# Performance work log

Measured on AMD Instinct MI355X. Metric: run time of the kernel, lower is better.

The kernel has to match this reference:

```python
import jax, jax.numpy as jnp
import numpy as np
from jax import lax

N = 10000
E = 320000
FLAT = 32 * 10 * 32  # conv channels * pooled 20x64 -> 10x32


def setup_inputs() -> dict:
    key = jax.random.key(0)
    ks = jax.random.split(key, 16)
    s = 0.05
    return {
        "features": jax.random.normal(ks[0], (N, 20, 64), jnp.float32),
        "src": jax.random.randint(ks[1], (E,), 0, N, jnp.int32),
        "dst": jax.random.randint(ks[2], (E,), 0, N, jnp.int32),
        # CNN params
        "conv_w": jax.random.normal(ks[3], (32, 1, 3, 3), jnp.float32) * s,
        "conv_b": jnp.zeros((32,), jnp.float32),
        "w1": jax.random.normal(ks[4], (FLAT, 32), jnp.float32) * s,
        "b1": jnp.zeros((32,), jnp.float32),
        "w2": jax.random.normal(ks[5], (32, 32), jnp.float32) * s,
        "b2": jnp.zeros((32,), jnp.float32),
        # SAGEConv1 (32 -> 64)
        "s1_self": jax.random.normal(ks[6], (32, 64), jnp.float32) * s,
        "s1_neigh": jax.random.normal(ks[7], (32, 64), jnp.float32) * s,
        "s1_b": jnp.zeros((64,), jnp.float32),
        # SAGEConv2 (64 -> 10)
        "s2_self": jax.random.normal(ks[8], (64, 10), jnp.float32) * s,
        "s2_neigh": jax.random.normal(ks[9], (64, 10), jnp.float32) * s,
        "s2_b": jnp.zeros((10,), jnp.float32),
    }


def _cnn(x, conv_w, conv_b, w1, b1, w2, b2):
    # x: [N, 1, 20, 64]
    x = lax.conv_general_dilated(x, conv_w, (1, 1), "SAME",
                                 dimension_numbers=("NCHW", "OIHW", "NCHW"))
    x = jax.nn.relu(x + conv_b[None, :, None, None])
    x = lax.reduce_window(x, -jnp.inf, lax.max, (1, 1, 2, 2), (1, 1, 2, 2), "VALID")
    x = x.reshape(x.shape[0], -1)  # [N, FLAT], NCHW flatten matches torch
    x = jax.nn.relu(x @ w1 + b1)
    x = jax.nn.relu(x @ w2 + b2)
    return x


def _sage_mean(x, src, dst, w_self, w_neigh, b):
    # DGL SAGEConv 'mean': mean over in-neighbors (messages src->dst)
    agg = jax.ops.segment_sum(x[src], dst, num_segments=N)
    deg = jax.ops.segment_sum(jnp.ones((src.shape[0],), x.dtype), dst, num_segments=N)
    agg = agg / jnp.maximum(deg, 1.0)[:, None]
    return x @ w_self + agg @ w_neigh + b


def reference(features, src, dst, conv_w, conv_b, w1, b1, w2, b2,
              s1_self, s1_neigh, s1_b, s2_self, s2_neigh, s2_b):
    h = _cnn(features[:, None, :, :], conv_w, conv_b, w1, b1, w2, b2)  # [N, 32]
    h = jax.nn.relu(_sage_mean(h, src, dst, s1_self, s1_neigh, s1_b))  # [N, 64]
    out = _sage_mean(h, src, dst, s2_self, s2_neigh, s2_b)             # [N, 10]
    return out
```

## Files before the change

kernel.cpp:

```cpp
#include <hip/hip_runtime.h>


typedef __attribute__((ext_vector_type(8)))  short bf16x8;
typedef __attribute__((ext_vector_type(4)))  float f32x4;
typedef __attribute__((ext_vector_type(16))) float f32x16;

__device__ __forceinline__ unsigned short f2bf(float v) {
    union { float f; unsigned int u; } x; x.f = v;
    unsigned int r = x.u + 0x7FFFu + ((x.u >> 16) & 1u);
    return (unsigned short)(r >> 16);
}
__device__ __forceinline__ float bf2f(unsigned short b) {
    union { float f; unsigned int u; } x; x.u = ((unsigned int)b) << 16;
    return x.f;
}
__device__ __forceinline__ unsigned cvtpk(float a, float b) {
    unsigned r;
    asm("v_cvt_pk_bf16_f32 %0, %1, %2" : "=v"(r) : "v"(a), "v"(b));
    return r;
}
__device__ __forceinline__ float lo2f(unsigned p) { union { unsigned u; float f; } x; x.u = p << 16; return x.f; }
__device__ __forceinline__ float hi2f(unsigned p) { union { unsigned u; float f; } x; x.u = p & 0xffff0000u; return x.f; }
__device__ __forceinline__ void split_pair(float a, float b, unsigned& hp, unsigned& lp) {
    hp = cvtpk(a, b);
    lp = cvtpk(a - lo2f(hp), b - hi2f(hp));
}

__global__ __launch_bounds__(256) void zero_ws(float* __restrict__ ws, int count) {
    int i = blockIdx.x * 256 + threadIdx.x;
    if (i < count) ws[i] = 0.0f;
}

__global__ __launch_bounds__(256) void w1_prep_v3(
    const float* __restrict__ w1, unsigned char* __restrict__ w1f)
{
    int gu = blockIdx.x * 256 + threadIdx.x;
    const int quarter = gu >> 11;
    const int u = gu & 2047;
    const int ph = quarter >> 2, qq = quarter & 3;
    const int ks   = u >> 8;
    const int jh   = (u >> 7) & 1;
    const int part = (u >> 6) & 1;
    const int lane = u & 63;
    const int j    = jh * 16 + (lane & 15);
    const int c    = ks * 4 + (lane >> 4);
    const int k0   = c * 320 + ph * 32 + qq * 8;
    unsigned short v[8];
#pragma unroll
    for (int i = 0; i < 8; ++i) {
        float x = w1[(size_t)(k0 + i) * 32 + j];
        unsigned short h = f2bf(x);
        v[i] = part ? f2bf(x - bf2f(h)) : h;
    }
    *(uint4*)(w1f + (size_t)quarter * 32768 + (size_t)u * 16) = *(const uint4*)v;
}

__global__ __launch_bounds__(256, 3) void cnn_fused_v10(
    const float* __restrict__ feat,
    const float* __restrict__ conv_w, const float* __restrict__ conv_b,
    const unsigned char* __restrict__ w1f,
    float* __restrict__ h_fc1)
{
    __shared__ __align__(16) unsigned char convA[18432];
    __shared__ __align__(16) unsigned char fc1A[32768];

    const int t = threadIdx.x;
    const int wv = t >> 6;
    const int lane = t & 63;
    const int base = blockIdx.x * 16;
    const int qq = blockIdx.y;

    const int nn  = lane >> 4;
    const int pwl = lane & 7;
    const int aa  = (lane >> 3) & 1;
    const float* featn = feat + (size_t)(base + wv * 4 + nn) * 1280;

    const int pw = qq * 8 + pwl;
    const int c0 = 2 * pw - 1;
    const bool cv0 = (c0 >= 0);
    const bool cv3 = (c0 + 3 < 64);

    const int cch = lane & 31;
    const int ckg = lane >> 5;
    const int rowr = lane & 31;
    unsigned rsw = (unsigned)(rowr << 4); rsw ^= ((rsw >> 7) & 3u) << 4;

    bf16x8 cbh, cbl;
    {
        union { unsigned short u[8]; bf16x8 v; } H, L;
#pragma unroll
        for (int i = 0; i < 8; ++i) {
            int k = ckg * 8 + i;
            float x = (k < 9) ? conv_w[cch * 9 + k] : 0.0f;
            unsigned short h = f2bf(x);
            H.u[i] = h; L.u[i] = f2bf(x - bf2f(h));
        }
        cbh = H.v; cbl = L.v;
    }
    const float cbias = conv_b[cch];

    const int nfr = lane & 15;

    f32x4 acc0 = {0.f, 0.f, 0.f, 0.f};
    f32x4 acc1 = {0.f, 0.f, 0.f, 0.f};
    const f32x16 czero = {};

    float f0[4], f1[4], f2[4], g1[4], g2[4];
    auto load_row = [&](int r, float* o) {
        bool rv = (r >= 0) && (r < 20);
        const float* rp = featn + (rv ? r : 0) * 64;
        float2 m = *(const float2*)(rp + c0 + 1);
        float v0 = rp[cv0 ? c0 : 0];
        float v3 = rp[cv3 ? (c0 + 3) : 0];
        o[0] = (rv && cv0) ? v0 : 0.f;
        o[1] = rv ? m.x : 0.f;
        o[2] = rv ? m.y : 0.f;
        o[3] = (rv && cv3) ? v3 : 0.f;
    };

    load_row(aa - 1, f0);
    load_row(aa,     f1);
    load_row(aa + 1, f2);
    load_row(aa + 2, g1);
    load_row(aa + 3, g2);

#pragma unroll
    for (int ph = 0; ph < 10; ++ph) {
        const int quarter = ph * 4 + qq;
        unsigned char* fbuf = fc1A + ((ph & 1) << 14);

        const unsigned char* wq = w1f + (size_t)quarter * 32768;
        bf16x8 bF[2][2][2];
#pragma unroll
        for (int si = 0; si < 2; ++si) {
            const int ks = wv + si * 4;
#pragma unroll
            for (int jh = 0; jh < 2; ++jh)
#pragma unroll
                for (int part = 0; part < 2; ++part)
                    bF[si][jh][part] = *(const bf16x8*)(
                        wq + (size_t)((((ks * 2 + jh) * 2 + part)) << 10) + lane * 16);
        }

        {
            unsigned P[3][2], Q[3][2];
            split_pair(f0[0], f0[1], P[0][0], Q[0][0]);
            split_pair(f0[2], f0[3], P[0][1], Q[0][1]);
            split_pair(f1[0], f1[1], P[1][0], Q[1][0]);
            split_pair(f1[2], f1[3], P[1][1], Q[1][1]);
            split_pair(f2[0], f2[1], P[2][0], Q[2][0]);
            split_pair(f2[2], f2[3], P[2][1], Q[2][1]);

            const int r0 = pwl * 4 + aa * 2, r1 = r0 + 1;
            unsigned b0 = (unsigned)(r0 << 4); b0 ^= ((b0 >> 7) & 3u) << 4;
            unsigned b1 = (unsigned)(r1 << 4); b1 ^= ((b1 >> 7) & 3u) << 4;
            unsigned char* abw = convA + ((wv * 4 + nn) << 10);
            uint4 H0 = make_uint4(P[0][0],
                                  __builtin_amdgcn_perm(P[1][0], P[0][1], 0x05040100u),
                                  __builtin_amdgcn_perm(P[1][1], P[1][0], 0x05040302u),
                                  P[2][0]);
            uint4 H1 = make_uint4(__builtin_amdgcn_perm(P[0][1], P[0][0], 0x05040302u),
                                  __builtin_amdgcn_perm(P[1][0], P[0][1], 0x07060302u),
                                  P[1][1],
                                  __builtin_amdgcn_perm(P[2][1], P[2][0], 0x05040302u));
            uint4 L0 = make_uint4(Q[0][0],
                                  __builtin_amdgcn_perm(Q[1][0], Q[0][1], 0x05040100u),
                                  __builtin_amdgcn_perm(Q[1][1], Q[1][0], 0x05040302u),
                                  Q[2][0]);
            uint4 L1 = make_uint4(__builtin_amdgcn_perm(Q[0][1], Q[0][0], 0x05040302u),
                                  __builtin_amdgcn_perm(Q[1][0], Q[0][1], 0x07060302u),
                                  Q[1][1],
                                  __builtin_amdgcn_perm(Q[2][1], Q[2][0], 0x05040302u));
            *(uint4*)(abw + b0)       = H0;
            *(uint4*)(abw + b1)       = H1;
            *(uint4*)(abw + 512 + b0) = L0;
            *(uint4*)(abw + 512 + b1) = L1;
            unsigned wr0 = __builtin_amdgcn_perm(Q[2][1], P[2][1], 0x05040100u);
            unsigned wr1 = __builtin_amdgcn_perm(Q[2][1], P[2][1], 0x07060302u);
            *(uint2*)(convA + 16384 + (((wv * 4 + nn) * 32 + r0) << 2)) = make_uint2(wr0, wr1);
        }

        if (ph < 9) {
#pragma unroll
            for (int j = 0; j < 4; ++j) { f0[j] = f2[j]; f1[j] = g1[j]; f2[j] = g2[j]; }
        }
        if (ph < 8) {
            load_row(2 * ph + 4 + aa, g1);
            load_row(2 * ph + 5 + aa, g2);
        }

#pragma unroll
        for (int nn2 = 0; nn2 < 4; ++nn2) {
            bf16x8 a_h, a_l;
            if (ckg == 0) {
                const unsigned char* ab = convA + ((wv * 4 + nn2) << 10);
                a_h = *(const bf16x8*)(ab + rsw);
                a_l = *(const bf16x8*)(ab + 512 + rsw);
            } else {
                unsigned cw = *(const unsigned*)(convA + 16384 + (((wv * 4 + nn2) * 32 + rowr) << 2));
                a_h = (bf16x8){(short)(cw & 0xffffu), 0, 0, 0, 0, 0, 0, 0};
                a_l = (bf16x8){(short)(cw >> 16),     0, 0, 0, 0, 0, 0, 0};
            }
            f32x16 ca;
            ca = __builtin_amdgcn_mfma_f32_32x32x16_bf16(a_l, cbh, czero, 0, 0, 0);
            ca = __builtin_amdgcn_mfma_f32_32x32x16_bf16(a_h, cbl, ca, 0, 0, 0);
            ca = __builtin_amdgcn_mfma_f32_32x32x16_bf16(a_h, cbh, ca, 0, 0, 0);

            float pv0 = fmaxf(fmaxf(fmaxf(ca[0],  ca[1]),  fmaxf(ca[2],  ca[3]))  + cbias, 0.f);
            float pv1 = fmaxf(fmaxf(fmaxf(ca[4],  ca[5]),  fmaxf(ca[6],  ca[7]))  + cbias, 0.f);
            float pv2 = fmaxf(fmaxf(fmaxf(ca[8],  ca[9]),  fmaxf(ca[10], ca[11])) + cbias, 0.f);
            float pv3 = fmaxf(fmaxf(fmaxf(ca[12], ca[13]), fmaxf(ca[14], ca[15])) + cbias, 0.f);

            unsigned ha, la, hb, lb;
            split_pair(pv0, pv1, ha, la);
            split_pair(pv2, pv3, hb, lb);
            unsigned pha = (unsigned)__shfl_xor((int)ha, 32);
            unsigned phb = (unsigned)__shfl_xor((int)hb, 32);
            unsigned pla = (unsigned)__shfl_xor((int)la, 32);
            unsigned plb = (unsigned)__shfl_xor((int)lb, 32);
            bool hih = (lane < 32);
            unsigned q0v = hih ? pha : la;
            unsigned q1v = hih ? ha  : pla;
            unsigned q2v = hih ? phb : lb;
            unsigned q3v = hih ? hb  : plb;
            unsigned w0  = __builtin_amdgcn_perm(q0v, q1v, 0x05040100u);
            unsigned w1v = __builtin_amdgcn_perm(q0v, q1v, 0x07060302u);
            unsigned w2v = __builtin_amdgcn_perm(q2v, q3v, 0x05040100u);
            unsigned w3v = __builtin_amdgcn_perm(q2v, q3v, 0x07060302u);
            const int nloc = wv * 4 + nn2;
            const int pS = hih ? 0 : 1;
            const int ksW = cch >> 2, kgW = cch & 3;
            unsigned byteW = (unsigned)((((pS * 8 + ksW) * 64) + kgW * 16 + nloc) << 4);
            byteW ^= ((byteW >> 8) & 7u) << 4;
            *(uint4*)(fbuf + byteW) = make_uint4(w0, w1v, w2v, w3v);
        }

        __syncthreads();

#pragma unroll
        for (int si = 0; si < 2; ++si) {
            const int ks = wv + si * 4;
            unsigned bH = (unsigned)(((0 * 8 + ks) << 10) + lane * 16); bH ^= ((bH >> 8) & 7u) << 4;
            unsigned bL = (unsigned)(((1 * 8 + ks) << 10) + lane * 16); bL ^= ((bL >> 8) & 7u) << 4;
            bf16x8 fa_h = *(const bf16x8*)(fbuf + bH);
            bf16x8 fa_l = *(const bf16x8*)(fbuf + bL);
            acc0 = __builtin_amdgcn_mfma_f32_16x16x32_bf16(fa_l, bF[si][0][0], acc0, 0, 0, 0);
            acc0 = __builtin_amdgcn_mfma_f32_16x16x32_bf16(fa_h, bF[si][0][1], acc0, 0, 0, 0);
            acc0 = __builtin_amdgcn_mfma_f32_16x16x32_bf16(fa_h, bF[si][0][0], acc0, 0, 0, 0);
            acc1 = __builtin_amdgcn_mfma_f32_16x16x32_bf16(fa_l, bF[si][1][0], acc1, 0, 0, 0);
            acc1 = __builtin_amdgcn_mfma_f32_16x16x32_bf16(fa_h, bF[si][1][1], acc1, 0, 0, 0);
            acc1 = __builtin_amdgcn_mfma_f32_16x16x32_bf16(fa_h, bF[si][1][0], acc1, 0, 0, 0);
        }
    }

    __syncthreads();
    float* red = (float*)convA;
#pragma unroll
    for (int r = 0; r < 4; ++r) {
        int node = (lane >> 4) * 4 + r;
        red[wv * 512 + node * 32 + nfr]      = acc0[r];
        red[wv * 512 + node * 32 + 16 + nfr] = acc1[r];
    }
    __syncthreads();
    {
        const int en = t >> 4, jp = t & 15;
        const int j0 = 2 * jp;
        float s0 = 0.f, s1 = 0.f;
#pragma unroll
        for (int wi = 0; wi < 4; ++wi) {
            s0 += red[wi * 512 + en * 32 + j0];
            s1 += red[wi * 512 + en * 32 + j0 + 1];
        }
        atomicAdd(&h_fc1[(size_t)(base + en) * 32 + j0],     s0);
        atomicAdd(&h_fc1[(size_t)(base + en) * 32 + j0 + 1], s1);
    }
}

__global__ __launch_bounds__(256) void fc1_finish(
    const float* __restrict__ h_fc1, const float* __restrict__ b1,
    const float* __restrict__ w2, const float* __restrict__ b2,
    float* __restrict__ h_out, int N)
{
    __shared__ float hr[8][32];
    const int t = threadIdx.x;
    const int nb = t >> 5, j = t & 31;
    const int n = blockIdx.x * 8 + nb;
    if (n < N) hr[nb][j] = fmaxf(h_fc1[(size_t)n * 32 + j] + b1[j], 0.f);
    __syncthreads();
    if (n >= N) return;
    float o = b2[j];
#pragma unroll
    for (int k = 0; k < 32; ++k) o = fmaf(hr[nb][k], w2[k * 32 + j], o);
    h_out[(size_t)n * 32 + j] = fmaxf(o, 0.f);
}

__global__ __launch_bounds__(256) void count_deg(
    const int* __restrict__ dst, int* __restrict__ cnt, int E)
{
    int e = blockIdx.x * 256 + threadIdx.x;
    if (e < E) atomicAdd(&cnt[dst[e]], 1);
}

__global__ __launch_bounds__(256) void scan_all(
    const int* __restrict__ cnt, int* __restrict__ row_ptr, int* __restrict__ cursor, int N)
{
    __shared__ int ps[256];
    const int t = threadIdx.x;
    const int base = t * 40;
    int vals[40];
    int run = 0;
#pragma unroll
    for (int i = 0; i < 40; ++i) {
        int idx = base + i;
        int v = (idx < N) ? cnt[idx] : 0;
        vals[i] = run;
        run += v;
    }
    ps[t] = run;
    __syncthreads();
#pragma unroll
    for (int off = 1; off < 256; off <<= 1) {
        int x = (t >= off) ? ps[t - off] : 0;
        __syncthreads();
        ps[t] += x;
        __syncthreads();
    }
    int excl = ps[t] - run;
#pragma unroll
    for (int i = 0; i < 40; ++i) {
        int idx = base + i;
        if (idx < N) {
            int rp = excl + vals[i];
            row_ptr[idx] = rp;
            cursor[idx]  = rp;
        }
    }
    if (t == 255) row_ptr[N] = ps[255];
}

__global__ __launch_bounds__(256) void fill_csr(
    const int* __restrict__ src, const int* __restrict__ dst,
    int* __restrict__ cursor, int* __restrict__ csr, int E)
{
    int e = blockIdx.x * 256 + threadIdx.x;
    if (e >= E) return;
    int idx = atomicAdd(&cursor[dst[e]], 1);
    csr[idx] = src[e];
}

__global__ __launch_bounds__(256) void sage1_fused(
    const float* __restrict__ h, const int* __restrict__ rp, const int* __restrict__ csr,
    const float* __restrict__ s1_self, const float* __restrict__ s1_neigh,
    const float* __restrict__ s1_b, const float* __restrict__ s2_neigh,
    float* __restrict__ h1, float* __restrict__ z16, int N)
{
    __shared__ float aggs[4][32];
    __shared__ float hl[4][64];
    const int t = threadIdx.x;
    const int nb = t >> 6, k = t & 63;
    const int n = blockIdx.x * 4 + nb;
    const int j = k & 31, half = k >> 5;

    int p0 = 0, p1 = 0;
    if (n < N) { p0 = rp[n]; p1 = rp[n + 1]; }
    float a = 0.f;
    for (int p = p0 + half; p < p1; p += 2)
        a += h[(size_t)csr[p] * 32 + j];
    a += __shfl_down(a, 32);
    if (half == 0) aggs[nb][j] = a;
    __syncthreads();

    float o = 0.f;
    if (n < N) {
        const int nu = __builtin_amdgcn_readfirstlane(n);
        float inv = 1.0f / fmaxf((float)(p1 - p0), 1.0f);
        o = s1_b[k];
#pragma unroll
        for (int jj = 0; jj < 32; ++jj) {
            o = fmaf(h[(size_t)nu * 32 + jj], s1_self[jj * 64 + k], o);
            o = fmaf(aggs[nb][jj] * inv, s1_neigh[jj * 64 + k], o);
        }
        o = fmaxf(o, 0.f);
        h1[(size_t)n * 64 + k] = o;
    }
    hl[nb][k] = o;
    __syncthreads();

    if (n < N && k < 16) {
        float z = 0.f;
        if (k < 10) {
#pragma unroll
            for (int jj = 0; jj < 64; ++jj) z = fmaf(hl[nb][jj], s2_neigh[jj * 10 + k], z);
        }
        z16[(size_t)n * 16 + k] = z;
    }
}

__global__ __launch_bounds__(256) void sage2_final_g(
    const float* __restrict__ h1, const float* __restrict__ z16,
    const int* __restrict__ rp, const int* __restrict__ csr,
    const float* __restrict__ s2_self, const float* __restrict__ s2_b,
    float* __restrict__ out, int N)
{
    int tid = blockIdx.x * 256 + threadIdx.x;
    int nn = tid >> 4, k = tid & 15;
    if (nn >= N || k >= 10) return;
    int p0 = rp[nn], p1 = rp[nn + 1];
    float a0 = 0.f, a1 = 0.f;
    int p = p0;
    for (; p + 2 <= p1; p += 2) {
        int s0 = csr[p], s1 = csr[p + 1];
        a0 += z16[(size_t)s0 * 16 + k];
        a1 += z16[(size_t)s1 * 16 + k];
    }
    if (p < p1) a0 += z16[(size_t)csr[p] * 16 + k];
    float inv = 1.0f / fmaxf((float)(p1 - p0), 1.0f);
    float o = s2_b[k] + (a0 + a1) * inv;
#pragma unroll
    for (int j = 0; j < 64; ++j) o = fmaf(h1[nn * 64 + j], s2_self[j * 10 + k], o);
    out[nn * 10 + k] = o;
}

extern "C" void kernel_launch(void* const* d_in, const int* in_sizes, int n_in,
                              void* d_out, int out_size, void* d_ws, size_t ws_size,
                              hipStream_t stream)
{
    const float* feat     = (const float*)d_in[0];
    const int*   src      = (const int*)d_in[1];
    const int*   dst      = (const int*)d_in[2];
    const float* conv_w   = (const float*)d_in[3];
    const float* conv_b   = (const float*)d_in[4];
    const float* w1       = (const float*)d_in[5];
    const float* b1       = (const float*)d_in[6];
    const float* w2       = (const float*)d_in[7];
    const float* b2       = (const float*)d_in[8];
    const float* s1_self  = (const float*)d_in[9];
    const float* s1_neigh = (const float*)d_in[10];
    const float* s1_b     = (const float*)d_in[11];
    const float* s2_self  = (const float*)d_in[12];
    const float* s2_neigh = (const float*)d_in[13];
    const float* s2_b     = (const float*)d_in[14];
    float* out = (float*)d_out;

    const int N = in_sizes[0] / 1280;
    const int E = in_sizes[1];

    char* wsb = (char*)d_ws;
    int*   row_cnt = (int*)wsb;                      wsb += (size_t)N * 4;
    float* h_fc1   = (float*)wsb;                    wsb += (size_t)N * 32 * 4;
    int*   row_ptr = (int*)wsb;                      wsb += (size_t)(N + 4) * 4;
    int*   cursor  = (int*)wsb;                      wsb += (size_t)N * 4;
    int*   csr     = (int*)wsb;                      wsb += (size_t)E * 4;
    float* h_cnn   = (float*)wsb;                    wsb += (size_t)N * 32 * 4;
    float* h1      = (float*)wsb;                    wsb += (size_t)N * 64 * 4;
    float* z16     = (float*)wsb;                    wsb += (size_t)N * 16 * 4;
    unsigned char* w1f = (unsigned char*)wsb;

    zero_ws<<<(33 * N + 255) / 256, 256, 0, stream>>>((float*)row_cnt, 33 * N);

    count_deg<<<(E + 255) / 256, 256, 0, stream>>>(dst, row_cnt, E);
    scan_all<<<1, 256, 0, stream>>>(row_cnt, row_ptr, cursor, N);
    fill_csr<<<(E + 255) / 256, 256, 0, stream>>>(src, dst, cursor, csr, E);

    w1_prep_v3<<<320, 256, 0, stream>>>(w1, w1f);
    dim3 cg(N / 16, 4);
    cnn_fused_v10<<<cg, 256, 0, stream>>>(feat, conv_w, conv_b, w1f, h_fc1);
    fc1_finish<<<(N + 7) / 8, 256, 0, stream>>>(h_fc1, b1, w2, b2, h_cnn, N);

    sage1_fused<<<(N + 3) / 4, 256, 0, stream>>>(
        h_cnn, row_ptr, csr, s1_self, s1_neigh, s1_b, s2_neigh, h1, z16, N);

    sage2_final_g<<<(int)(((size_t)N * 16 + 255) / 256), 256, 0, stream>>>(
        h1, z16, row_ptr, csr, s2_self, s2_b, out, N);
}
```

Before: 211.1 us.

## Merge prep kernels, use memset, stop unrolling CNN loop, pack sage2 threads

The zero kernel becomes hipMemsetAsync, and degree counting is merged with the w1 prep kernel into one launch, cutting launch count. The CNN phase loop is no longer unrolled and no longer prefetches rows two phases ahead, which lowers register pressure and code size but exposes feature-load latency. sage2_final_g now maps ten threads per node instead of sixteen, so no lanes sit idle.

```diff
diff --git a/kernel.cpp b/kernel.cpp
--- a/kernel.cpp
+++ b/kernel.cpp
@@ -26,15 +26,17 @@
     lp = cvtpk(a - lo2f(hp), b - hi2f(hp));
 }
 
-__global__ __launch_bounds__(256) void zero_ws(float* __restrict__ ws, int count) {
-    int i = blockIdx.x * 256 + threadIdx.x;
-    if (i < count) ws[i] = 0.0f;
-}
-
-__global__ __launch_bounds__(256) void w1_prep_v3(
+__global__ __launch_bounds__(256) void prep_merged(
+    const int* __restrict__ dst, int* __restrict__ cnt, int E, int nb_cnt,
     const float* __restrict__ w1, unsigned char* __restrict__ w1f)
 {
-    int gu = blockIdx.x * 256 + threadIdx.x;
+    const int b = blockIdx.x;
+    if (b < nb_cnt) {
+        int e = b * 256 + threadIdx.x;
+        if (e < E) atomicAdd(&cnt[dst[e]], 1);
+        return;
+    }
+    int gu = (b - nb_cnt) * 256 + threadIdx.x;
     const int quarter = gu >> 11;
     const int u = gu & 2047;
     const int ph = quarter >> 2, qq = quarter & 3;
@@ -55,7 +57,7 @@
     *(uint4*)(w1f + (size_t)quarter * 32768 + (size_t)u * 16) = *(const uint4*)v;
 }
 
-__global__ __launch_bounds__(256, 3) void cnn_fused_v10(
+__global__ __launch_bounds__(256, 3) void cnn_fused_v11(
     const float* __restrict__ feat,
     const float* __restrict__ conv_w, const float* __restrict__ conv_b,
     const unsigned char* __restrict__ w1f,
@@ -105,7 +107,7 @@
     f32x4 acc1 = {0.f, 0.f, 0.f, 0.f};
     const f32x16 czero = {};
 
-    float f0[4], f1[4], f2[4], g1[4], g2[4];
+    float f0[4], f1[4], f2[4];
     auto load_row = [&](int r, float* o) {
         bool rv = (r >= 0) && (r < 20);
         const float* rp = featn + (rv ? r : 0) * 64;
@@ -121,10 +123,8 @@
     load_row(aa - 1, f0);
     load_row(aa,     f1);
     load_row(aa + 1, f2);
-    load_row(aa + 2, g1);
-    load_row(aa + 3, g2);
-
-#pragma unroll
+
+#pragma unroll 1
     for (int ph = 0; ph < 10; ++ph) {
         const int quarter = ph * 4 + qq;
         unsigned char* fbuf = fc1A + ((ph & 1) << 14);
@@ -182,11 +182,9 @@
 
         if (ph < 9) {
 #pragma unroll
-            for (int j = 0; j < 4; ++j) { f0[j] = f2[j]; f1[j] = g1[j]; f2[j] = g2[j]; }
-        }
-        if (ph < 8) {
-            load_row(2 * ph + 4 + aa, g1);
-            load_row(2 * ph + 5 + aa, g2);
+            for (int j = 0; j < 4; ++j) f0[j] = f2[j];
+            load_row(2 * ph + 2 + aa, f1);
+            load_row(2 * ph + 3 + aa, f2);
         }
 
 #pragma unroll
@@ -294,13 +292,6 @@
     h_out[(size_t)n * 32 + j] = fmaxf(o, 0.f);
 }
 
-__global__ __launch_bounds__(256) void count_deg(
-    const int* __restrict__ dst, int* __restrict__ cnt, int E)
-{
-    int e = blockIdx.x * 256 + threadIdx.x;
-    if (e < E) atomicAdd(&cnt[dst[e]], 1);
-}
-
 __global__ __launch_bounds__(256) void scan_all(
     const int* __restrict__ cnt, int* __restrict__ row_ptr, int* __restrict__ cursor, int N)
 {
@@ -403,8 +394,9 @@
     float* __restrict__ out, int N)
 {
     int tid = blockIdx.x * 256 + threadIdx.x;
-    int nn = tid >> 4, k = tid & 15;
-    if (nn >= N || k >= 10) return;
+    int nn = tid / 10;
+    int k = tid - nn * 10;
+    if (nn >= N) return;
     int p0 = rp[nn], p1 = rp[nn + 1];
     float a0 = 0.f, a1 = 0.f;
     int p = p0;
@@ -444,6 +436,7 @@
 
     const int N = in_sizes[0] / 1280;
     const int E = in_sizes[1];
+    const int NB_CNT = (E + 255) / 256;
 
     char* wsb = (char*)d_ws;
     int*   row_cnt = (int*)wsb;                      wsb += (size_t)N * 4;
@@ -456,20 +449,20 @@
     float* z16     = (float*)wsb;                    wsb += (size_t)N * 16 * 4;
     unsigned char* w1f = (unsigned char*)wsb;
 
-    zero_ws<<<(33 * N + 255) / 256, 256, 0, stream>>>((float*)row_cnt, 33 * N);
-
-    count_deg<<<(E + 255) / 256, 256, 0, stream>>>(dst, row_cnt, E);
+    hipMemsetAsync(row_cnt, 0, (size_t)33 * N * 4, stream);
+
+    prep_merged<<<NB_CNT + 320, 256, 0, stream>>>(dst, row_cnt, E, NB_CNT, w1, w1f);
+
     scan_all<<<1, 256, 0, stream>>>(row_cnt, row_ptr, cursor, N);
-    fill_csr<<<(E + 255) / 256, 256, 0, stream>>>(src, dst, cursor, csr, E);
-
-    w1_prep_v3<<<320, 256, 0, stream>>>(w1, w1f);
+    fill_csr<<<NB_CNT, 256, 0, stream>>>(src, dst, cursor, csr, E);
+
     dim3 cg(N / 16, 4);
-    cnn_fused_v10<<<cg, 256, 0, stream>>>(feat, conv_w, conv_b, w1f, h_fc1);
+    cnn_fused_v11<<<cg, 256, 0, stream>>>(feat, conv_w, conv_b, w1f, h_fc1);
     fc1_finish<<<(N + 7) / 8, 256, 0, stream>>>(h_fc1, b1, w2, b2, h_cnn, N);
 
     sage1_fused<<<(N + 3) / 4, 256, 0, stream>>>(
         h_cnn, row_ptr, csr, s1_self, s1_neigh, s1_b, s2_neigh, h1, z16, N);
 
-    sage2_final_g<<<(int)(((size_t)N * 16 + 255) / 256), 256, 0, stream>>>(
+    sage2_final_g<<<(int)(((size_t)N * 10 + 255) / 256), 256, 0, stream>>>(
         h1, z16, row_ptr, csr, s2_self, s2_b, out, N);
 }
```

Measured after the change: 219.2 us. 1.04x slower.
